# Kernel optimization log

Measured on AMD Instinct MI355X. Metric: run time of the kernel, lower is better.

Reference implementation:

```python
import jax, jax.numpy as jnp
import numpy as np

N_NODES = 100000


def setup_inputs() -> dict:
    key = jax.random.key(0)
    k1, k2, k3 = jax.random.split(key, 3)
    x = jax.random.normal(k1, (N_NODES, 64), dtype=jnp.float32)
    edge_index = jax.random.randint(k2, (2, 3200000), 0, N_NODES, dtype=jnp.int64)
    W = jax.random.normal(k3, (64, 64), dtype=jnp.float32) * (1.0 / np.sqrt(64.0))
    b = jnp.zeros((64,), dtype=jnp.float32)
    return {"x": x, "edge_index": edge_index, "W": W, "b": b}


def reference(x, edge_index, W, b):
    # GCNConv (PyG semantics): add self-loops, symmetric normalization,
    # linear transform, scatter-add aggregation, bias.
    n = x.shape[0]
    loops = jnp.arange(n, dtype=edge_index.dtype)
    src = jnp.concatenate([edge_index[0], loops])  # [E+N]
    dst = jnp.concatenate([edge_index[1], loops])  # [E+N]

    # degree of destination nodes (counts incoming edges incl. self-loops)
    ones = jnp.ones(dst.shape[0], dtype=x.dtype)
    deg = jax.ops.segment_sum(ones, dst, num_segments=n)  # [N]
    deg_inv_sqrt = jnp.where(deg > 0, jax.lax.rsqrt(deg), 0.0)
    norm = deg_inv_sqrt[src] * deg_inv_sqrt[dst]  # [E+N]

    h = x @ W.T  # [N, 64] linear transform first (PyG order)
    msg = h[src] * norm[:, None]  # gather + scale, [E+N, 64]
    out = jax.ops.segment_sum(msg, dst, num_segments=n)  # scatter-add
    return out + b
```

## Files before the change

kernel.cpp:

```cpp
#include <hip/hip_runtime.h>
#include <hip/hip_fp16.h>


#define NB 8
#define NR 128
#define CAP 4096
#define CSTR 32
#define NPB 128
#define FCAP 4608
#define FSTR 32

typedef __attribute__((ext_vector_type(8))) _Float16 f16x8;
typedef __attribute__((ext_vector_type(4))) float f32x4;

__global__ void bin_k(const int* __restrict__ ei, int* __restrict__ cnt,
                      unsigned* __restrict__ pairs, int E, int nper) {
    int lane = threadIdx.x & 63;
    int rep = ((blockIdx.x & 7) << 4) | ((blockIdx.x >> 3) & 15);
    long gw = ((long)blockIdx.x * blockDim.x + threadIdx.x) >> 6;
    long nw = ((long)gridDim.x * blockDim.x) >> 6;
    for (long base = gw * 64; base < E; base += nw * 64) {
        long e = base + lane;
        int bkt = -1, s = 0, d = 0;
        if (e < E) {
            d = __builtin_nontemporal_load(ei + E + e);
            s = __builtin_nontemporal_load(ei + e);
            bkt = d / nper;
        }
#pragma unroll
        for (int k = 0; k < NB; ++k) {
            unsigned long long mask = __ballot(bkt == k);
            if (mask) {
                int leader = (int)__ffsll((long long)mask) - 1;
                int pos0 = 0;
                if (lane == leader)
                    pos0 = atomicAdd(&cnt[(k * NR + rep) * CSTR], __popcll(mask));
                pos0 = __shfl(pos0, leader, 64);
                if (bkt == k) {
                    int idx = pos0 + (int)__popcll(mask & ((1ull << lane) - 1));
                    if (idx < CAP)
                        pairs[((size_t)k * NR + rep) * CAP + idx] =
                            ((unsigned)s << 14) | (unsigned)(d - k * nper);
                }
            }
        }
    }
}

__global__ void finebin_k(const unsigned* __restrict__ pairs, const int* __restrict__ cnt,
                          int* __restrict__ fcur, unsigned* __restrict__ fseg,
                          int nper) {
    __shared__ int lcnt[104];
    __shared__ int lofs[104];
    __shared__ int lpos[104];
    __shared__ int gbase[104];
    __shared__ unsigned stage[CAP];
    int b = blockIdx.x & 7;
    int rep = blockIdx.x >> 3;
    int t = threadIdx.x;
    int len = cnt[(b * NR + rep) * CSTR];
    if (len > CAP) len = CAP;
    const unsigned* p = pairs + ((size_t)b * NR + rep) * CAP;
    int nbase = b * nper;
    int fb0 = nbase / NPB;
    int nfl = (nbase + nper - 1) / NPB - fb0 + 1;

    for (int i = t; i < 104; i += 256) lcnt[i] = 0;
    __syncthreads();

    unsigned rec[16];
#pragma unroll
    for (int k = 0; k < 16; ++k) {
        int i = t + k * 256;
        unsigned v = 0xFFFFFFFFu;
        if (i < len) {
            v = p[i];
            int n = nbase + (int)(v & 16383u);
            atomicAdd(&lcnt[(n >> 7) - fb0], 1);
        }
        rec[k] = v;
    }
    __syncthreads();

    if (t < 104) lofs[t] = lcnt[t];
    __syncthreads();
    for (int off = 1; off < 104; off <<= 1) {
        int add = (t >= off && t < 104) ? lofs[t - off] : 0;
        __syncthreads();
        if (t < 104) lofs[t] += add;
        __syncthreads();
    }
    if (t < 104) {
        int e = lofs[t] - lcnt[t];
        lofs[t] = e;
        lpos[t] = e;
        if (t < nfl && lcnt[t] > 0)
            gbase[t] = atomicAdd(&fcur[(fb0 + t) * FSTR], lcnt[t]);
    }
    __syncthreads();

#pragma unroll
    for (int k = 0; k < 16; ++k) {
        unsigned v = rec[k];
        if (v != 0xFFFFFFFFu) {
            int n = nbase + (int)(v & 16383u);
            int fl = (n >> 7) - fb0;
            int pos = atomicAdd(&lpos[fl], 1);
            stage[pos] = ((unsigned)fl << 24) | ((v >> 14) << 7) | (unsigned)(n & 127);
        }
    }
    __syncthreads();

    for (int i = t; i < len; i += 256) {
        unsigned w = stage[i];
        int fl = (int)(w >> 24);
        int gaddr = gbase[fl] + (i - lofs[fl]);
        if (gaddr < FCAP)
            fseg[(size_t)(fb0 + fl) * FCAP + gaddr] = w & 0xFFFFFFu;
    }
}

__global__ void sort2_k(const unsigned* __restrict__ fseg, const int* __restrict__ fcur,
                        int* __restrict__ ent, int* __restrict__ nodeoff,
                        int* __restrict__ deg, float* __restrict__ dis, int N) {
    __shared__ int lcnt[NPB];
    __shared__ int lofs[NPB];
    __shared__ int lpos[NPB];
    __shared__ unsigned stage[FCAP];
    int f = blockIdx.x;
    int t = threadIdx.x;
    int len = fcur[f * FSTR];
    if (len > FCAP) len = FCAP;
    const unsigned* p = fseg + (size_t)f * FCAP;

    if (t < NPB) lcnt[t] = 0;
    __syncthreads();
#pragma unroll
    for (int k = 0; k < 18; ++k) {
        int i = t + k * 256;
        if (i < len) atomicAdd(&lcnt[p[i] & 127u], 1);
    }
    __syncthreads();
    if (t < NPB) lofs[t] = lcnt[t];
    __syncthreads();
    for (int off = 1; off < NPB; off <<= 1) {
        int add = (t >= off && t < NPB) ? lofs[t - off] : 0;
        __syncthreads();
        if (t < NPB) lofs[t] += add;
        __syncthreads();
    }
    if (t < NPB) {
        int e = lofs[t] - lcnt[t];
        lofs[t] = e;
        lpos[t] = e;
    }
    __syncthreads();
#pragma unroll
    for (int k = 0; k < 18; ++k) {
        int i = t + k * 256;
        if (i < len) {
            unsigned v = p[i];
            int pos = atomicAdd(&lpos[v & 127u], 1);
            stage[pos] = v >> 7;
        }
    }
    __syncthreads();
    for (int i = t; i < len; i += 256)
        ent[(size_t)f * FCAP + i] = (int)stage[i];
    if (t < NPB) {
        int n = f * NPB + t;
        if (n < N) {
            nodeoff[n] = lofs[t];
            deg[n] = lcnt[t];
            dis[n] = rsqrtf((float)(lcnt[t] + 1));
        }
    }
}

__global__ void transform_k(const float* __restrict__ x, const float* __restrict__ W,
                            const float* __restrict__ dis, __half* __restrict__ h, int N) {
    int lane = threadIdx.x & 63;
    int wid = blockIdx.x * (blockDim.x >> 6) + (threadIdx.x >> 6);
    long row0 = (long)wid * 16;
    if (row0 >= N) return;
    int lr = lane & 15;
    int lk = lane >> 4;

    f16x8 bf[4][2];
#pragma unroll
    for (int ct = 0; ct < 4; ++ct)
#pragma unroll
        for (int kh = 0; kh < 2; ++kh) {
            const float* wp = W + (lr + 16 * ct) * 64 + lk * 8 + 32 * kh;
            f16x8 tv;
#pragma unroll
            for (int j = 0; j < 8; ++j) tv[j] = (_Float16)wp[j];
            bf[ct][kh] = tv;
        }

    const float* xp = x + (row0 + lr) * 64 + lk * 8;
    f16x8 af[2];
#pragma unroll
    for (int kh = 0; kh < 2; ++kh) {
        f16x8 tv;
#pragma unroll
        for (int j = 0; j < 8; ++j) tv[j] = (_Float16)xp[j + 32 * kh];
        af[kh] = tv;
    }

    float ds[4];
#pragma unroll
    for (int r = 0; r < 4; ++r) ds[r] = dis[row0 + lk * 4 + r];

#pragma unroll
    for (int ct = 0; ct < 4; ++ct) {
        f32x4 acc = {0.0f, 0.0f, 0.0f, 0.0f};
        acc = __builtin_amdgcn_mfma_f32_16x16x32_f16(af[0], bf[ct][0], acc, 0, 0, 0);
        acc = __builtin_amdgcn_mfma_f32_16x16x32_f16(af[1], bf[ct][1], acc, 0, 0, 0);
#pragma unroll
        for (int r = 0; r < 4; ++r) {
            long rr = row0 + lk * 4 + r;
            h[rr * 64 + lr + 16 * ct] = __float2half(acc[r] * ds[r]);
        }
    }
}

__global__ void gather_k(const int* __restrict__ nodeoff, const int* __restrict__ deg,
                         const int* __restrict__ ent, const float* __restrict__ dis,
                         const __half* __restrict__ h, const float* __restrict__ b,
                         float* __restrict__ out, int N) {
    int lane = threadIdx.x & 63;
    int n = blockIdx.x * (blockDim.x >> 6) + (threadIdx.x >> 6);
    if (n >= N) return;
    const __half* hl = h + lane;
    float acc = __half2float(hl[(long)n * 64]);
    int f = n >> 7;
    const int* lst = ent + (size_t)f * FCAP + nodeoff[n];
    int dg = deg[n];
    for (int i = 0; i < dg; i += 64) {
        int m = dg - i;
        if (m > 64) m = 64;
        int src = (lane < m) ? lst[i + lane] : 0;
        int j = 0;
        for (; j + 16 <= m; j += 16) {
            int s0  = __builtin_amdgcn_readlane(src, j + 0);
            int s1  = __builtin_amdgcn_readlane(src, j + 1);
            int s2  = __builtin_amdgcn_readlane(src, j + 2);
            int s3  = __builtin_amdgcn_readlane(src, j + 3);
            int s4  = __builtin_amdgcn_readlane(src, j + 4);
            int s5  = __builtin_amdgcn_readlane(src, j + 5);
            int s6  = __builtin_amdgcn_readlane(src, j + 6);
            int s7  = __builtin_amdgcn_readlane(src, j + 7);
            int s8  = __builtin_amdgcn_readlane(src, j + 8);
            int s9  = __builtin_amdgcn_readlane(src, j + 9);
            int s10 = __builtin_amdgcn_readlane(src, j + 10);
            int s11 = __builtin_amdgcn_readlane(src, j + 11);
            int s12 = __builtin_amdgcn_readlane(src, j + 12);
            int s13 = __builtin_amdgcn_readlane(src, j + 13);
            int s14 = __builtin_amdgcn_readlane(src, j + 14);
            int s15 = __builtin_amdgcn_readlane(src, j + 15);
            float v0  = __half2float(hl[(long)s0  * 64]);
            float v1  = __half2float(hl[(long)s1  * 64]);
            float v2  = __half2float(hl[(long)s2  * 64]);
            float v3  = __half2float(hl[(long)s3  * 64]);
            float v4  = __half2float(hl[(long)s4  * 64]);
            float v5  = __half2float(hl[(long)s5  * 64]);
            float v6  = __half2float(hl[(long)s6  * 64]);
            float v7  = __half2float(hl[(long)s7  * 64]);
            float v8  = __half2float(hl[(long)s8  * 64]);
            float v9  = __half2float(hl[(long)s9  * 64]);
            float v10 = __half2float(hl[(long)s10 * 64]);
            float v11 = __half2float(hl[(long)s11 * 64]);
            float v12 = __half2float(hl[(long)s12 * 64]);
            float v13 = __half2float(hl[(long)s13 * 64]);
            float v14 = __half2float(hl[(long)s14 * 64]);
            float v15 = __half2float(hl[(long)s15 * 64]);
            acc += (((v0 + v1) + (v2 + v3)) + ((v4 + v5) + (v6 + v7)))
                 + (((v8 + v9) + (v10 + v11)) + ((v12 + v13) + (v14 + v15)));
        }
        for (; j + 4 <= m; j += 4) {
            int s0 = __builtin_amdgcn_readlane(src, j + 0);
            int s1 = __builtin_amdgcn_readlane(src, j + 1);
            int s2 = __builtin_amdgcn_readlane(src, j + 2);
            int s3 = __builtin_amdgcn_readlane(src, j + 3);
            float v0 = __half2float(hl[(long)s0 * 64]);
            float v1 = __half2float(hl[(long)s1 * 64]);
            float v2 = __half2float(hl[(long)s2 * 64]);
            float v3 = __half2float(hl[(long)s3 * 64]);
            acc += (v0 + v1) + (v2 + v3);
        }
        for (; j < m; ++j) {
            int s = __builtin_amdgcn_readlane(src, j);
            acc += __half2float(hl[(long)s * 64]);
        }
    }
    __builtin_nontemporal_store(acc * dis[n] + b[lane], out + (long)n * 64 + lane);
}

extern "C" void kernel_launch(void* const* d_in, const int* in_sizes, int n_in,
                              void* d_out, int out_size, void* d_ws, size_t ws_size,
                              hipStream_t stream) {
    const float* x  = (const float*)d_in[0];
    const int*   ei = (const int*)d_in[1];
    const float* W  = (const float*)d_in[2];
    const float* b  = (const float*)d_in[3];
    float* out = (float*)d_out;

    int N = in_sizes[0] / 64;
    int E = in_sizes[1] / 2;
    int nper = (N + NB - 1) / NB;
    int nft = (N + NPB - 1) / NPB;

    char* ws = (char*)d_ws;
    size_t off = 0;
    auto alloc = [&](size_t bytes) { char* p = ws + off; off += (bytes + 255) & ~(size_t)255; return p; };
    int*      cnt     = (int*)alloc((size_t)NB * NR * CSTR * 4);
    unsigned* pairs   = (unsigned*)alloc((size_t)NB * NR * CAP * 4);
    int*      fcur    = (int*)alloc((size_t)nft * FSTR * 4);
    unsigned* fseg    = (unsigned*)alloc((size_t)nft * FCAP * 4);
    int*      nodeoff = (int*)alloc((size_t)N * 4);
    int*      deg     = (int*)alloc((size_t)N * 4);
    float*    dis     = (float*)alloc((size_t)N * 4);
    __half*   h       = (__half*)alloc((size_t)N * 64 * 2);
    int*      ent     = (int*)pairs;

    hipMemsetAsync(cnt, 0, (size_t)NB * NR * CSTR * 4, stream);
    hipMemsetAsync(fcur, 0, (size_t)nft * FSTR * 4, stream);
    bin_k<<<2048, 256, 0, stream>>>(ei, cnt, pairs, E, nper);
    finebin_k<<<NB * NR, 256, 0, stream>>>(pairs, cnt, fcur, fseg, nper);
    sort2_k<<<nft, 256, 0, stream>>>(fseg, fcur, ent, nodeoff, deg, dis, N);
    int nwave = (N + 15) / 16;
    transform_k<<<(nwave + 3) / 4, 256, 0, stream>>>(x, W, dis, h, N);
    gather_k<<<(N + 3) / 4, 256, 0, stream>>>(nodeoff, deg, ent, dis, h, b, out, N);
}
```

Measured before the change: 157.9 us.

## Gather two neighbor rows per wave using half2 loads; merge memsets

The gather kernel now splits each 64-lane wave into two half-waves. Each half-wave loads a different neighbor's row as 32 half2 values, and the two partial sums are combined with a shuffle at the end. This doubles the bytes per load instruction and halves the number of dependent load iterations per neighbor list, at the cost of extra shuffles and tail handling for odd degrees. The two workspace memsets are also merged into one by placing the buffers next to each other, saving one launch.

```diff
diff --git a/kernel.cpp b/kernel.cpp
--- a/kernel.cpp
+++ b/kernel.cpp
@@ -12,6 +12,7 @@
 
 typedef __attribute__((ext_vector_type(8))) _Float16 f16x8;
 typedef __attribute__((ext_vector_type(4))) float f32x4;
+typedef __attribute__((ext_vector_type(2))) float f32x2;
 
 __global__ void bin_k(const int* __restrict__ ei, int* __restrict__ cnt,
                       unsigned* __restrict__ pairs, int E, int nper) {
@@ -230,71 +231,82 @@
                          const __half* __restrict__ h, const float* __restrict__ b,
                          float* __restrict__ out, int N) {
     int lane = threadIdx.x & 63;
+    int hi = lane >> 5;
+    int c = lane & 31;
     int n = blockIdx.x * (blockDim.x >> 6) + (threadIdx.x >> 6);
     if (n >= N) return;
-    const __half* hl = h + lane;
-    float acc = __half2float(hl[(long)n * 64]);
+    const __half2* h2 = (const __half2*)h;
+
+    float acc0 = 0.0f, acc1 = 0.0f;
+    {
+        __half2 sv = h2[(long)n * 32 + c];
+        if (!hi) { acc0 = __low2float(sv); acc1 = __high2float(sv); }
+    }
+
     int f = n >> 7;
     const int* lst = ent + (size_t)f * FCAP + nodeoff[n];
     int dg = deg[n];
+
+#define PAIR_LOAD(T, P) __half2 T = h2[(long)__shfl(src, 2 * (P) + hi, 64) * 32 + c]
+#define PAIR_ACC2(A, B) acc0 += __low2float(A) + __low2float(B); \
+                        acc1 += __high2float(A) + __high2float(B)
+
     for (int i = 0; i < dg; i += 64) {
         int m = dg - i;
         if (m > 64) m = 64;
-        int src = (lane < m) ? lst[i + lane] : 0;
-        int j = 0;
-        for (; j + 16 <= m; j += 16) {
-            int s0  = __builtin_amdgcn_readlane(src, j + 0);
-            int s1  = __builtin_amdgcn_readlane(src, j + 1);
-            int s2  = __builtin_amdgcn_readlane(src, j + 2);
-            int s3  = __builtin_amdgcn_readlane(src, j + 3);
-            int s4  = __builtin_amdgcn_readlane(src, j + 4);
-            int s5  = __builtin_amdgcn_readlane(src, j + 5);
-            int s6  = __builtin_amdgcn_readlane(src, j + 6);
-            int s7  = __builtin_amdgcn_readlane(src, j + 7);
-            int s8  = __builtin_amdgcn_readlane(src, j + 8);
-            int s9  = __builtin_amdgcn_readlane(src, j + 9);
-            int s10 = __builtin_amdgcn_readlane(src, j + 10);
-            int s11 = __builtin_amdgcn_readlane(src, j + 11);
-            int s12 = __builtin_amdgcn_readlane(src, j + 12);
-            int s13 = __builtin_amdgcn_readlane(src, j + 13);
-            int s14 = __builtin_amdgcn_readlane(src, j + 14);
-            int s15 = __builtin_amdgcn_readlane(src, j + 15);
-            float v0  = __half2float(hl[(long)s0  * 64]);
-            float v1  = __half2float(hl[(long)s1  * 64]);
-            float v2  = __half2float(hl[(long)s2  * 64]);
-            float v3  = __half2float(hl[(long)s3  * 64]);
-            float v4  = __half2float(hl[(long)s4  * 64]);
-            float v5  = __half2float(hl[(long)s5  * 64]);
-            float v6  = __half2float(hl[(long)s6  * 64]);
-            float v7  = __half2float(hl[(long)s7  * 64]);
-            float v8  = __half2float(hl[(long)s8  * 64]);
-            float v9  = __half2float(hl[(long)s9  * 64]);
-            float v10 = __half2float(hl[(long)s10 * 64]);
-            float v11 = __half2float(hl[(long)s11 * 64]);
-            float v12 = __half2float(hl[(long)s12 * 64]);
-            float v13 = __half2float(hl[(long)s13 * 64]);
-            float v14 = __half2float(hl[(long)s14 * 64]);
-            float v15 = __half2float(hl[(long)s15 * 64]);
-            acc += (((v0 + v1) + (v2 + v3)) + ((v4 + v5) + (v6 + v7)))
-                 + (((v8 + v9) + (v10 + v11)) + ((v12 + v13) + (v14 + v15)));
-        }
-        for (; j + 4 <= m; j += 4) {
-            int s0 = __builtin_amdgcn_readlane(src, j + 0);
-            int s1 = __builtin_amdgcn_readlane(src, j + 1);
-            int s2 = __builtin_amdgcn_readlane(src, j + 2);
-            int s3 = __builtin_amdgcn_readlane(src, j + 3);
-            float v0 = __half2float(hl[(long)s0 * 64]);
-            float v1 = __half2float(hl[(long)s1 * 64]);
-            float v2 = __half2float(hl[(long)s2 * 64]);
-            float v3 = __half2float(hl[(long)s3 * 64]);
-            acc += (v0 + v1) + (v2 + v3);
-        }
-        for (; j < m; ++j) {
-            int s = __builtin_amdgcn_readlane(src, j);
-            acc += __half2float(hl[(long)s * 64]);
-        }
-    }
-    __builtin_nontemporal_store(acc * dis[n] + b[lane], out + (long)n * 64 + lane);
+        int src = (lane < m) ? __builtin_nontemporal_load(lst + i + lane) : 0;
+        int mp = m >> 1;
+        int p = 0;
+        for (; p + 16 <= mp; p += 16) {
+            PAIR_LOAD(v0, p + 0);  PAIR_LOAD(v1, p + 1);
+            PAIR_LOAD(v2, p + 2);  PAIR_LOAD(v3, p + 3);
+            PAIR_LOAD(v4, p + 4);  PAIR_LOAD(v5, p + 5);
+            PAIR_LOAD(v6, p + 6);  PAIR_LOAD(v7, p + 7);
+            PAIR_LOAD(v8, p + 8);  PAIR_LOAD(v9, p + 9);
+            PAIR_LOAD(v10, p + 10); PAIR_LOAD(v11, p + 11);
+            PAIR_LOAD(v12, p + 12); PAIR_LOAD(v13, p + 13);
+            PAIR_LOAD(v14, p + 14); PAIR_LOAD(v15, p + 15);
+            PAIR_ACC2(v0, v1);   PAIR_ACC2(v2, v3);
+            PAIR_ACC2(v4, v5);   PAIR_ACC2(v6, v7);
+            PAIR_ACC2(v8, v9);   PAIR_ACC2(v10, v11);
+            PAIR_ACC2(v12, v13); PAIR_ACC2(v14, v15);
+        }
+        for (; p + 8 <= mp; p += 8) {
+            PAIR_LOAD(v0, p + 0);  PAIR_LOAD(v1, p + 1);
+            PAIR_LOAD(v2, p + 2);  PAIR_LOAD(v3, p + 3);
+            PAIR_LOAD(v4, p + 4);  PAIR_LOAD(v5, p + 5);
+            PAIR_LOAD(v6, p + 6);  PAIR_LOAD(v7, p + 7);
+            PAIR_ACC2(v0, v1); PAIR_ACC2(v2, v3);
+            PAIR_ACC2(v4, v5); PAIR_ACC2(v6, v7);
+        }
+        for (; p + 4 <= mp; p += 4) {
+            PAIR_LOAD(v0, p + 0); PAIR_LOAD(v1, p + 1);
+            PAIR_LOAD(v2, p + 2); PAIR_LOAD(v3, p + 3);
+            PAIR_ACC2(v0, v1); PAIR_ACC2(v2, v3);
+        }
+        for (; p < mp; ++p) {
+            PAIR_LOAD(v0, p);
+            acc0 += __low2float(v0);
+            acc1 += __high2float(v0);
+        }
+        if (m & 1) {
+            __half2 tv = h2[(long)__shfl(src, (m - 1) + hi, 64) * 32 + c];
+            if (!hi) { acc0 += __low2float(tv); acc1 += __high2float(tv); }
+        }
+    }
+#undef PAIR_LOAD
+#undef PAIR_ACC2
+
+    float o0 = __shfl(acc0, c + 32, 64);
+    float o1 = __shfl(acc1, c + 32, 64);
+    if (!hi) {
+        float dn = dis[n];
+        const float* bp = b + 2 * c;
+        f32x2 r;
+        r.x = (acc0 + o0) * dn + bp[0];
+        r.y = (acc1 + o1) * dn + bp[1];
+        __builtin_nontemporal_store(r, (f32x2*)(out + (long)n * 64 + 2 * c));
+    }
 }
 
 extern "C" void kernel_launch(void* const* d_in, const int* in_sizes, int n_in,
@@ -315,8 +327,8 @@
     size_t off = 0;
     auto alloc = [&](size_t bytes) { char* p = ws + off; off += (bytes + 255) & ~(size_t)255; return p; };
     int*      cnt     = (int*)alloc((size_t)NB * NR * CSTR * 4);
+    int*      fcur    = (int*)alloc((size_t)nft * FSTR * 4);
     unsigned* pairs   = (unsigned*)alloc((size_t)NB * NR * CAP * 4);
-    int*      fcur    = (int*)alloc((size_t)nft * FSTR * 4);
     unsigned* fseg    = (unsigned*)alloc((size_t)nft * FCAP * 4);
     int*      nodeoff = (int*)alloc((size_t)N * 4);
     int*      deg     = (int*)alloc((size_t)N * 4);
@@ -324,8 +336,7 @@
     __half*   h       = (__half*)alloc((size_t)N * 64 * 2);
     int*      ent     = (int*)pairs;
 
-    hipMemsetAsync(cnt, 0, (size_t)NB * NR * CSTR * 4, stream);
-    hipMemsetAsync(fcur, 0, (size_t)nft * FSTR * 4, stream);
+    (void)hipMemsetAsync(cnt, 0, (size_t)((char*)fcur - (char*)cnt) + (size_t)nft * FSTR * 4, stream);
     bin_k<<<2048, 256, 0, stream>>>(ei, cnt, pairs, E, nper);
     finebin_k<<<NB * NR, 256, 0, stream>>>(pairs, cnt, fcur, fseg, nper);
     sort2_k<<<nft, 256, 0, stream>>>(fseg, fcur, ent, nodeoff, deg, dis, N);
```

After: 168.8 us. 1.07x slower.

## Fuse per-tile sort with gather aggregation, add lightweight degree kernel

Applied to the files above, without the earlier changes.

The per-tile counting sort is merged into the gather kernel. Each 512-thread block now sorts its 128-node tile's edges in shared memory and aggregates directly from LDS, so the sorted edge list and the per-node offset and degree arrays no longer make a round trip through global memory. A separate small kernel computes degrees and dis before the transform, which means fseg is read twice. The two memsets are merged into one by making the workspace regions adjacent. The risk is coarser parallelism: one block per tile with 8 waves each handling 16 nodes, which may lower occupancy and latency hiding for the random gathers.

```diff
diff --git a/kernel.cpp b/kernel.cpp
--- a/kernel.cpp
+++ b/kernel.cpp
@@ -120,9 +120,77 @@
     }
 }
 
-__global__ void sort2_k(const unsigned* __restrict__ fseg, const int* __restrict__ fcur,
-                        int* __restrict__ ent, int* __restrict__ nodeoff,
-                        int* __restrict__ deg, float* __restrict__ dis, int N) {
+__global__ void degdis_k(const unsigned* __restrict__ fseg, const int* __restrict__ fcur,
+                         float* __restrict__ dis, int N) {
+    __shared__ int lcnt[NPB];
+    int f = blockIdx.x;
+    int t = threadIdx.x;
+    if (t < NPB) lcnt[t] = 0;
+    __syncthreads();
+    int len = fcur[f * FSTR];
+    if (len > FCAP) len = FCAP;
+    const unsigned* p = fseg + (size_t)f * FCAP;
+    for (int i = t; i < len; i += 256)
+        atomicAdd(&lcnt[p[i] & 127u], 1);
+    __syncthreads();
+    if (t < NPB) {
+        int n = f * NPB + t;
+        if (n < N) dis[n] = rsqrtf((float)(lcnt[t] + 1));
+    }
+}
+
+__global__ void transform_k(const float* __restrict__ x, const float* __restrict__ W,
+                            const float* __restrict__ dis, __half* __restrict__ h, int N) {
+    int lane = threadIdx.x & 63;
+    int wid = blockIdx.x * (blockDim.x >> 6) + (threadIdx.x >> 6);
+    long row0 = (long)wid * 16;
+    if (row0 >= N) return;
+    int lr = lane & 15;
+    int lk = lane >> 4;
+
+    f16x8 bf[4][2];
+#pragma unroll
+    for (int ct = 0; ct < 4; ++ct)
+#pragma unroll
+        for (int kh = 0; kh < 2; ++kh) {
+            const float* wp = W + (lr + 16 * ct) * 64 + lk * 8 + 32 * kh;
+            f16x8 tv;
+#pragma unroll
+            for (int j = 0; j < 8; ++j) tv[j] = (_Float16)wp[j];
+            bf[ct][kh] = tv;
+        }
+
+    const float* xp = x + (row0 + lr) * 64 + lk * 8;
+    f16x8 af[2];
+#pragma unroll
+    for (int kh = 0; kh < 2; ++kh) {
+        f16x8 tv;
+#pragma unroll
+        for (int j = 0; j < 8; ++j) tv[j] = (_Float16)xp[j + 32 * kh];
+        af[kh] = tv;
+    }
+
+    float ds[4];
+#pragma unroll
+    for (int r = 0; r < 4; ++r) ds[r] = dis[row0 + lk * 4 + r];
+
+#pragma unroll
+    for (int ct = 0; ct < 4; ++ct) {
+        f32x4 acc = {0.0f, 0.0f, 0.0f, 0.0f};
+        acc = __builtin_amdgcn_mfma_f32_16x16x32_f16(af[0], bf[ct][0], acc, 0, 0, 0);
+        acc = __builtin_amdgcn_mfma_f32_16x16x32_f16(af[1], bf[ct][1], acc, 0, 0, 0);
+#pragma unroll
+        for (int r = 0; r < 4; ++r) {
+            long rr = row0 + lk * 4 + r;
+            h[rr * 64 + lr + 16 * ct] = __float2half(acc[r] * ds[r]);
+        }
+    }
+}
+
+__global__ void __launch_bounds__(512)
+gs_k(const unsigned* __restrict__ fseg, const int* __restrict__ fcur,
+     const float* __restrict__ dis, const __half* __restrict__ h,
+     const float* __restrict__ b, float* __restrict__ out, int N) {
     __shared__ int lcnt[NPB];
     __shared__ int lofs[NPB];
     __shared__ int lpos[NPB];
@@ -135,11 +203,8 @@
 
     if (t < NPB) lcnt[t] = 0;
     __syncthreads();
-#pragma unroll
-    for (int k = 0; k < 18; ++k) {
-        int i = t + k * 256;
-        if (i < len) atomicAdd(&lcnt[p[i] & 127u], 1);
-    }
+    for (int i = t; i < len; i += 512)
+        atomicAdd(&lcnt[p[i] & 127u], 1);
     __syncthreads();
     if (t < NPB) lofs[t] = lcnt[t];
     __syncthreads();
@@ -155,146 +220,84 @@
         lpos[t] = e;
     }
     __syncthreads();
-#pragma unroll
-    for (int k = 0; k < 18; ++k) {
-        int i = t + k * 256;
-        if (i < len) {
-            unsigned v = p[i];
-            int pos = atomicAdd(&lpos[v & 127u], 1);
-            stage[pos] = v >> 7;
-        }
-    }
-    __syncthreads();
-    for (int i = t; i < len; i += 256)
-        ent[(size_t)f * FCAP + i] = (int)stage[i];
-    if (t < NPB) {
-        int n = f * NPB + t;
-        if (n < N) {
-            nodeoff[n] = lofs[t];
-            deg[n] = lcnt[t];
-            dis[n] = rsqrtf((float)(lcnt[t] + 1));
-        }
-    }
-}
-
-__global__ void transform_k(const float* __restrict__ x, const float* __restrict__ W,
-                            const float* __restrict__ dis, __half* __restrict__ h, int N) {
-    int lane = threadIdx.x & 63;
-    int wid = blockIdx.x * (blockDim.x >> 6) + (threadIdx.x >> 6);
-    long row0 = (long)wid * 16;
-    if (row0 >= N) return;
-    int lr = lane & 15;
-    int lk = lane >> 4;
-
-    f16x8 bf[4][2];
-#pragma unroll
-    for (int ct = 0; ct < 4; ++ct)
-#pragma unroll
-        for (int kh = 0; kh < 2; ++kh) {
-            const float* wp = W + (lr + 16 * ct) * 64 + lk * 8 + 32 * kh;
-            f16x8 tv;
-#pragma unroll
-            for (int j = 0; j < 8; ++j) tv[j] = (_Float16)wp[j];
-            bf[ct][kh] = tv;
-        }
-
-    const float* xp = x + (row0 + lr) * 64 + lk * 8;
-    f16x8 af[2];
-#pragma unroll
-    for (int kh = 0; kh < 2; ++kh) {
-        f16x8 tv;
-#pragma unroll
-        for (int j = 0; j < 8; ++j) tv[j] = (_Float16)xp[j + 32 * kh];
-        af[kh] = tv;
-    }
-
-    float ds[4];
-#pragma unroll
-    for (int r = 0; r < 4; ++r) ds[r] = dis[row0 + lk * 4 + r];
-
-#pragma unroll
-    for (int ct = 0; ct < 4; ++ct) {
-        f32x4 acc = {0.0f, 0.0f, 0.0f, 0.0f};
-        acc = __builtin_amdgcn_mfma_f32_16x16x32_f16(af[0], bf[ct][0], acc, 0, 0, 0);
-        acc = __builtin_amdgcn_mfma_f32_16x16x32_f16(af[1], bf[ct][1], acc, 0, 0, 0);
-#pragma unroll
-        for (int r = 0; r < 4; ++r) {
-            long rr = row0 + lk * 4 + r;
-            h[rr * 64 + lr + 16 * ct] = __float2half(acc[r] * ds[r]);
-        }
-    }
-}
-
-__global__ void gather_k(const int* __restrict__ nodeoff, const int* __restrict__ deg,
-                         const int* __restrict__ ent, const float* __restrict__ dis,
-                         const __half* __restrict__ h, const float* __restrict__ b,
-                         float* __restrict__ out, int N) {
-    int lane = threadIdx.x & 63;
-    int n = blockIdx.x * (blockDim.x >> 6) + (threadIdx.x >> 6);
-    if (n >= N) return;
+    for (int i = t; i < len; i += 512) {
+        unsigned v = p[i];
+        int pos = atomicAdd(&lpos[v & 127u], 1);
+        stage[pos] = v >> 7;
+    }
+    __syncthreads();
+
+    int lane = t & 63;
+    int w = t >> 6;
     const __half* hl = h + lane;
-    float acc = __half2float(hl[(long)n * 64]);
-    int f = n >> 7;
-    const int* lst = ent + (size_t)f * FCAP + nodeoff[n];
-    int dg = deg[n];
-    for (int i = 0; i < dg; i += 64) {
-        int m = dg - i;
-        if (m > 64) m = 64;
-        int src = (lane < m) ? lst[i + lane] : 0;
-        int j = 0;
-        for (; j + 16 <= m; j += 16) {
-            int s0  = __builtin_amdgcn_readlane(src, j + 0);
-            int s1  = __builtin_amdgcn_readlane(src, j + 1);
-            int s2  = __builtin_amdgcn_readlane(src, j + 2);
-            int s3  = __builtin_amdgcn_readlane(src, j + 3);
-            int s4  = __builtin_amdgcn_readlane(src, j + 4);
-            int s5  = __builtin_amdgcn_readlane(src, j + 5);
-            int s6  = __builtin_amdgcn_readlane(src, j + 6);
-            int s7  = __builtin_amdgcn_readlane(src, j + 7);
-            int s8  = __builtin_amdgcn_readlane(src, j + 8);
-            int s9  = __builtin_amdgcn_readlane(src, j + 9);
-            int s10 = __builtin_amdgcn_readlane(src, j + 10);
-            int s11 = __builtin_amdgcn_readlane(src, j + 11);
-            int s12 = __builtin_amdgcn_readlane(src, j + 12);
-            int s13 = __builtin_amdgcn_readlane(src, j + 13);
-            int s14 = __builtin_amdgcn_readlane(src, j + 14);
-            int s15 = __builtin_amdgcn_readlane(src, j + 15);
-            float v0  = __half2float(hl[(long)s0  * 64]);
-            float v1  = __half2float(hl[(long)s1  * 64]);
-            float v2  = __half2float(hl[(long)s2  * 64]);
-            float v3  = __half2float(hl[(long)s3  * 64]);
-            float v4  = __half2float(hl[(long)s4  * 64]);
-            float v5  = __half2float(hl[(long)s5  * 64]);
-            float v6  = __half2float(hl[(long)s6  * 64]);
-            float v7  = __half2float(hl[(long)s7  * 64]);
-            float v8  = __half2float(hl[(long)s8  * 64]);
-            float v9  = __half2float(hl[(long)s9  * 64]);
-            float v10 = __half2float(hl[(long)s10 * 64]);
-            float v11 = __half2float(hl[(long)s11 * 64]);
-            float v12 = __half2float(hl[(long)s12 * 64]);
-            float v13 = __half2float(hl[(long)s13 * 64]);
-            float v14 = __half2float(hl[(long)s14 * 64]);
-            float v15 = __half2float(hl[(long)s15 * 64]);
-            acc += (((v0 + v1) + (v2 + v3)) + ((v4 + v5) + (v6 + v7)))
-                 + (((v8 + v9) + (v10 + v11)) + ((v12 + v13) + (v14 + v15)));
-        }
-        for (; j + 4 <= m; j += 4) {
-            int s0 = __builtin_amdgcn_readlane(src, j + 0);
-            int s1 = __builtin_amdgcn_readlane(src, j + 1);
-            int s2 = __builtin_amdgcn_readlane(src, j + 2);
-            int s3 = __builtin_amdgcn_readlane(src, j + 3);
-            float v0 = __half2float(hl[(long)s0 * 64]);
-            float v1 = __half2float(hl[(long)s1 * 64]);
-            float v2 = __half2float(hl[(long)s2 * 64]);
-            float v3 = __half2float(hl[(long)s3 * 64]);
-            acc += (v0 + v1) + (v2 + v3);
-        }
-        for (; j < m; ++j) {
-            int s = __builtin_amdgcn_readlane(src, j);
-            acc += __half2float(hl[(long)s * 64]);
-        }
-    }
-    __builtin_nontemporal_store(acc * dis[n] + b[lane], out + (long)n * 64 + lane);
+    float bl = b[lane];
+#pragma unroll 1
+    for (int r = 0; r < 16; ++r) {
+        int d = w * 16 + r;
+        int n = f * NPB + d;
+        if (n >= N) break;
+        float acc = __half2float(hl[(long)n * 64]);
+        int beg = lofs[d];
+        int dg = lcnt[d];
+        for (int i = 0; i < dg; i += 64) {
+            int m = dg - i;
+            if (m > 64) m = 64;
+            unsigned src = (lane < m) ? stage[beg + i + lane] : 0;
+            int j = 0;
+            for (; j + 16 <= m; j += 16) {
+                unsigned s0  = __builtin_amdgcn_readlane(src, j + 0);
+                unsigned s1  = __builtin_amdgcn_readlane(src, j + 1);
+                unsigned s2  = __builtin_amdgcn_readlane(src, j + 2);
+                unsigned s3  = __builtin_amdgcn_readlane(src, j + 3);
+                unsigned s4  = __builtin_amdgcn_readlane(src, j + 4);
+                unsigned s5  = __builtin_amdgcn_readlane(src, j + 5);
+                unsigned s6  = __builtin_amdgcn_readlane(src, j + 6);
+                unsigned s7  = __builtin_amdgcn_readlane(src, j + 7);
+                unsigned s8  = __builtin_amdgcn_readlane(src, j + 8);
+                unsigned s9  = __builtin_amdgcn_readlane(src, j + 9);
+                unsigned s10 = __builtin_amdgcn_readlane(src, j + 10);
+                unsigned s11 = __builtin_amdgcn_readlane(src, j + 11);
+                unsigned s12 = __builtin_amdgcn_readlane(src, j + 12);
+                unsigned s13 = __builtin_amdgcn_readlane(src, j + 13);
+                unsigned s14 = __builtin_amdgcn_readlane(src, j + 14);
+                unsigned s15 = __builtin_amdgcn_readlane(src, j + 15);
+                float v0  = __half2float(hl[(long)s0  * 64]);
+                float v1  = __half2float(hl[(long)s1  * 64]);
+                float v2  = __half2float(hl[(long)s2  * 64]);
+                float v3  = __half2float(hl[(long)s3  * 64]);
+                float v4  = __half2float(hl[(long)s4  * 64]);
+                float v5  = __half2float(hl[(long)s5  * 64]);
+                float v6  = __half2float(hl[(long)s6  * 64]);
+                float v7  = __half2float(hl[(long)s7  * 64]);
+                float v8  = __half2float(hl[(long)s8  * 64]);
+                float v9  = __half2float(hl[(long)s9  * 64]);
+                float v10 = __half2float(hl[(long)s10 * 64]);
+                float v11 = __half2float(hl[(long)s11 * 64]);
+                float v12 = __half2float(hl[(long)s12 * 64]);
+                float v13 = __half2float(hl[(long)s13 * 64]);
+                float v14 = __half2float(hl[(long)s14 * 64]);
+                float v15 = __half2float(hl[(long)s15 * 64]);
+                acc += (((v0 + v1) + (v2 + v3)) + ((v4 + v5) + (v6 + v7)))
+                     + (((v8 + v9) + (v10 + v11)) + ((v12 + v13) + (v14 + v15)));
+            }
+            for (; j + 4 <= m; j += 4) {
+                unsigned s0 = __builtin_amdgcn_readlane(src, j + 0);
+                unsigned s1 = __builtin_amdgcn_readlane(src, j + 1);
+                unsigned s2 = __builtin_amdgcn_readlane(src, j + 2);
+                unsigned s3 = __builtin_amdgcn_readlane(src, j + 3);
+                float v0 = __half2float(hl[(long)s0 * 64]);
+                float v1 = __half2float(hl[(long)s1 * 64]);
+                float v2 = __half2float(hl[(long)s2 * 64]);
+                float v3 = __half2float(hl[(long)s3 * 64]);
+                acc += (v0 + v1) + (v2 + v3);
+            }
+            for (; j < m; ++j) {
+                unsigned s = __builtin_amdgcn_readlane(src, j);
+                acc += __half2float(hl[(long)s * 64]);
+            }
+        }
+        __builtin_nontemporal_store(acc * dis[n] + bl, out + (long)n * 64 + lane);
+    }
 }
 
 extern "C" void kernel_launch(void* const* d_in, const int* in_sizes, int n_in,
@@ -315,21 +318,17 @@
     size_t off = 0;
     auto alloc = [&](size_t bytes) { char* p = ws + off; off += (bytes + 255) & ~(size_t)255; return p; };
     int*      cnt     = (int*)alloc((size_t)NB * NR * CSTR * 4);
+    int*      fcur    = (int*)alloc((size_t)nft * FSTR * 4);
     unsigned* pairs   = (unsigned*)alloc((size_t)NB * NR * CAP * 4);
-    int*      fcur    = (int*)alloc((size_t)nft * FSTR * 4);
     unsigned* fseg    = (unsigned*)alloc((size_t)nft * FCAP * 4);
-    int*      nodeoff = (int*)alloc((size_t)N * 4);
-    int*      deg     = (int*)alloc((size_t)N * 4);
     float*    dis     = (float*)alloc((size_t)N * 4);
     __half*   h       = (__half*)alloc((size_t)N * 64 * 2);
-    int*      ent     = (int*)pairs;
-
-    hipMemsetAsync(cnt, 0, (size_t)NB * NR * CSTR * 4, stream);
-    hipMemsetAsync(fcur, 0, (size_t)nft * FSTR * 4, stream);
+
+    (void)hipMemsetAsync(cnt, 0, (size_t)((char*)fcur - (char*)cnt) + (size_t)nft * FSTR * 4, stream);
     bin_k<<<2048, 256, 0, stream>>>(ei, cnt, pairs, E, nper);
     finebin_k<<<NB * NR, 256, 0, stream>>>(pairs, cnt, fcur, fseg, nper);
-    sort2_k<<<nft, 256, 0, stream>>>(fseg, fcur, ent, nodeoff, deg, dis, N);
+    degdis_k<<<nft, 256, 0, stream>>>(fseg, fcur, dis, N);
     int nwave = (N + 15) / 16;
     transform_k<<<(nwave + 3) / 4, 256, 0, stream>>>(x, W, dis, h, N);
-    gather_k<<<(N + 3) / 4, 256, 0, stream>>>(nodeoff, deg, ent, dis, h, b, out, N);
-}
+    gs_k<<<nft, 512, 0, stream>>>(fseg, fcur, dis, h, b, out, N);
+}
```

After: 161.9 us. +2.6%, slower.
